# Kernel optimization log

Hardware: AMD Instinct MI355X
Metric: run time of the kernel (lower is better)

The kernel has to match this reference:

```python
import jax, jax.numpy as jnp
import numpy as np

NUM_HEADS = 16
EPS = 1e-6

def _ln(x):
    # LayerNorm32: no affine, eps=1e-6, computed in fp32
    x32 = x.astype(jnp.float32)
    mu = x32.mean(-1, keepdims=True)
    var = x32.var(-1, keepdims=True)
    return ((x32 - mu) * jax.lax.rsqrt(var + EPS)).astype(x.dtype)

def setup_inputs() -> dict:
    key = jax.random.key(0)
    ks = jax.random.split(key, 20)
    B, N, T, C = 2, 2048, 256, 1024
    H = 4 * C
    s = 0.02
    inp = {
        "x": jax.random.normal(ks[0], (B, N, C), jnp.float32),
        "mod": jax.random.normal(ks[1], (B, C), jnp.float32),
        "cond": jax.random.normal(ks[2], (B, T, C), jnp.float32),
        # adaLN: SiLU -> Linear(C, 6C)
        "w_adaln": jax.random.normal(ks[3], (C, 6 * C), jnp.float32) * s,
        "b_adaln": jnp.zeros((6 * C,), jnp.float32),
        # attention qkv + out proj
        "w_qkv": jax.random.normal(ks[4], (C, 3 * C), jnp.float32) * s,
        "b_qkv": jnp.zeros((3 * C,), jnp.float32),
        "w_proj": jax.random.normal(ks[5], (C, C), jnp.float32) * s,
        "b_proj": jnp.zeros((C,), jnp.float32),
        # sparse-branch MLP (GELU tanh)
        "w_s1": jax.random.normal(ks[6], (C, H), jnp.float32) * s,
        "b_s1": jnp.zeros((H,), jnp.float32),
        "w_s2": jax.random.normal(ks[7], (H, C), jnp.float32) * s,
        "b_s2": jnp.zeros((C,), jnp.float32),
        # dense cond MLP (SiLU)
        "w_d1": jax.random.normal(ks[8], (C, H), jnp.float32) * s,
        "b_d1": jnp.zeros((H,), jnp.float32),
        "w_d2": jax.random.normal(ks[9], (H, C), jnp.float32) * s,
        "b_d2": jnp.zeros((C,), jnp.float32),
    }
    return inp

def reference(x, mod, cond, w_adaln, b_adaln, w_qkv, b_qkv, w_proj, b_proj,
              w_s1, b_s1, w_s2, b_s2, w_d1, b_d1, w_d2, b_d2):
    B, N, C = x.shape
    T = cond.shape[1]
    D = C // NUM_HEADS

    # adaLN-zero modulation: [B, 6C] -> six [B, C]
    m = jax.nn.silu(mod) @ w_adaln + b_adaln
    sh_msa, sc_msa, g_msa, sh_mlp, sc_mlp, g_mlp = jnp.split(m, 6, axis=-1)

    # LN + (1+scale)*x + shift on both branches
    x_adaln = _ln(x) * (1.0 + sc_msa[:, None]) + sh_msa[:, None]
    c_adaln = _ln(cond) * (1.0 + sc_msa[:, None]) + sh_msa[:, None]

    # joint tokens per batch: [B, S, C], S = N + T (x tokens first, then cond)
    joint = jnp.concatenate([x_adaln, c_adaln], axis=1)
    S = N + T

    # full multi-head self-attention over the joint sequence
    qkv = joint @ w_qkv + b_qkv                       # [B, S, 3C]
    qkv = qkv.reshape(B, S, 3, NUM_HEADS, D)
    q, k, v = qkv[:, :, 0], qkv[:, :, 1], qkv[:, :, 2]  # [B, S, H, D]
    scores = jnp.einsum('bshd,bthd->bhst', q, k) / jnp.sqrt(jnp.asarray(D, q.dtype))
    attn = jax.nn.softmax(scores, axis=-1)
    out = jnp.einsum('bhst,bthd->bshd', attn, v).reshape(B, S, C)
    out = out @ w_proj + b_proj

    x_attn, c_attn = out[:, :N], out[:, N:]
    x = x + x_attn * g_msa[:, None]
    cond = cond + c_attn * g_msa[:, None]

    # sparse-branch MLP with adaLN (GELU tanh)
    x2 = _ln(x) * (1.0 + sc_mlp[:, None]) + sh_mlp[:, None]
    x2 = jax.nn.gelu(x2 @ w_s1 + b_s1, approximate=True) @ w_s2 + b_s2
    x = x + x2 * g_mlp[:, None]

    # dense cond MLP with adaLN (SiLU)
    c2 = _ln(cond) * (1.0 + sc_mlp[:, None]) + sh_mlp[:, None]
    c2 = jax.nn.silu(c2 @ w_d1 + b_d1) @ w_d2 + b_d2
    cond = cond + c2 * g_mlp[:, None]

    return (x, cond)
```

## Files before the change

kernel.cpp:

```cpp
#include <hip/hip_runtime.h>

typedef unsigned short u16;
typedef __attribute__((ext_vector_type(8))) short short8;
typedef __attribute__((ext_vector_type(4))) short s4b;
typedef __attribute__((ext_vector_type(4))) float floatx4;

#define S_TOT 2304
#define N_SEQ 2048
#define T_SEQ 256
#define C_DIM 1024
#define NH 16
#define DH 64
#define SIX_C 6144

__device__ __forceinline__ u16 f2bf(float f) {
  union { float f; unsigned u; } v; v.f = f;
  unsigned r = (v.u + 0x7FFFu + ((v.u >> 16) & 1u)) >> 16;
  return (u16)r;
}
__device__ __forceinline__ float bf2f(u16 u) {
  union { unsigned u; float f; } v; v.u = ((unsigned)u) << 16; return v.f;
}
__device__ __forceinline__ unsigned fbits(float f) {
  union { float f; unsigned u; } v; v.f = f; return v.u;
}

__device__ __forceinline__ void async16(const void* g, void* l) {
  __builtin_amdgcn_global_load_lds((const __attribute__((address_space(1))) void*)g,
                                   (__attribute__((address_space(3))) void*)l, 16, 0, 0);
}

__device__ __forceinline__ floatx4 zero4() {
  floatx4 z; z[0] = 0.f; z[1] = 0.f; z[2] = 0.f; z[3] = 0.f; return z;
}

__global__ __launch_bounds__(256)
void adaln_mod(const float* __restrict__ mod, const float* __restrict__ w,
               float* __restrict__ m) {
  __shared__ float sm[128];
  int b = blockIdx.y, kz = blockIdx.z;
  int tid = threadIdx.x;
  if (tid < 128) {
    float v = mod[b * C_DIM + kz * 128 + tid];
    sm[tid] = v / (1.f + __expf(-v));
  }
  __syncthreads();
  int j = blockIdx.x * 256 + tid;
  const float* wp = w + (size_t)(kz * 128) * SIX_C + j;
  float acc = 0.f;
  #pragma unroll 8
  for (int k = 0; k < 128; k++) acc += sm[k] * wp[(size_t)k * SIX_C];
  atomicAdd(&m[b * SIX_C + j], acc);
}

__global__ __launch_bounds__(256)
void wtrans_all(const float* __restrict__ w0, const float* __restrict__ w1,
                const float* __restrict__ w2, const float* __restrict__ w3,
                const float* __restrict__ w4, const float* __restrict__ w5,
                u16* __restrict__ o0, u16* __restrict__ o1, u16* __restrict__ o2,
                u16* __restrict__ o3, u16* __restrict__ o4, u16* __restrict__ o5) {
  int bid = blockIdx.x;
  const float* W; u16* Wt; int K, N, bx, local;
  if (bid < 3072)       { W = w0; Wt = o0; K = 1024; N = 3072; bx = 96;  local = bid; }
  else if (bid < 4096)  { W = w1; Wt = o1; K = 1024; N = 1024; bx = 32;  local = bid - 3072; }
  else if (bid < 8192)  { W = w2; Wt = o2; K = 1024; N = 4096; bx = 128; local = bid - 4096; }
  else if (bid < 12288) { W = w3; Wt = o3; K = 4096; N = 1024; bx = 32;  local = bid - 8192; }
  else if (bid < 16384) { W = w4; Wt = o4; K = 1024; N = 4096; bx = 128; local = bid - 12288; }
  else                  { W = w5; Wt = o5; K = 4096; N = 1024; bx = 32;  local = bid - 16384; }
  int n0 = (local % bx) << 5, k0 = (local / bx) << 5;
  __shared__ float t[32][33];
  int tx = threadIdx.x & 31, ty = threadIdx.x >> 5;
  #pragma unroll
  for (int i = 0; i < 32; i += 8)
    t[ty + i][tx] = W[(size_t)(k0 + ty + i) * N + n0 + tx];
  __syncthreads();
  #pragma unroll
  for (int i = 0; i < 32; i += 8)
    Wt[(size_t)(n0 + ty + i) * K + k0 + tx] = f2bf(t[tx][ty + i]);
}

__global__ __launch_bounds__(256)
void vtrans(const u16* __restrict__ V, u16* __restrict__ Vt) {
  __shared__ u16 t[64][65];
  int s0 = blockIdx.x << 6;
  int bh = blockIdx.y;
  const u16* src = V + (size_t)bh * S_TOT * DH;
  u16* dst = Vt + (size_t)bh * DH * S_TOT;
  int tid = threadIdx.x;
  #pragma unroll
  for (int i = 0; i < 16; i++) {
    int idx = tid + i * 256; int r = idx >> 6, c = idx & 63;
    t[r][c] = src[(size_t)(s0 + r) * DH + c];
  }
  __syncthreads();
  #pragma unroll
  for (int i = 0; i < 16; i++) {
    int idx = tid + i * 256; int r = idx >> 6, c = idx & 63;
    dst[(size_t)r * S_TOT + s0 + c] = t[c][r];
  }
}

template<int SHIFT_OFS>
__global__ __launch_bounds__(256)
void ln_mod(const float* __restrict__ xin, const float* __restrict__ cin,
            const float* __restrict__ m, const float* __restrict__ ba,
            u16* __restrict__ xo, u16* __restrict__ co, u16* __restrict__ joint) {
  int row = blockIdx.x;
  int b = row / S_TOT, s = row - b * S_TOT;
  bool isx = (s < N_SEQ);
  size_t roff = isx ? (((size_t)(b * N_SEQ + s)) << 10)
                    : (((size_t)(b * T_SEQ + (s - N_SEQ))) << 10);
  const float* src = isx ? (xin + roff) : (cin + roff);
  int tid = threadIdx.x;
  float4 v = ((const float4*)src)[tid];
  float s1 = v.x + v.y + v.z + v.w;
  float s2 = v.x * v.x + v.y * v.y + v.z * v.z + v.w * v.w;
  #pragma unroll
  for (int o = 32; o; o >>= 1) { s1 += __shfl_xor(s1, o); s2 += __shfl_xor(s2, o); }
  __shared__ float red[8];
  int wv = tid >> 6, ln = tid & 63;
  if (ln == 0) { red[wv] = s1; red[4 + wv] = s2; }
  __syncthreads();
  s1 = red[0] + red[1] + red[2] + red[3];
  s2 = red[4] + red[5] + red[6] + red[7];
  float mu = s1 * (1.f / 1024.f);
  float var = s2 * (1.f / 1024.f) - mu * mu;
  float rstd = rsqrtf(var + 1e-6f);
  int c = tid << 2;
  const float* mb = m + b * SIX_C;
  float4 sc = *(const float4*)(mb + SHIFT_OFS + 1024 + c);
  float4 sb = *(const float4*)(ba + SHIFT_OFS + 1024 + c);
  float4 sh = *(const float4*)(mb + SHIFT_OFS + c);
  float4 hb = *(const float4*)(ba + SHIFT_OFS + c);
  float y0 = (v.x - mu) * rstd * (1.f + sc.x + sb.x) + sh.x + hb.x;
  float y1 = (v.y - mu) * rstd * (1.f + sc.y + sb.y) + sh.y + hb.y;
  float y2 = (v.z - mu) * rstd * (1.f + sc.z + sb.z) + sh.z + hb.z;
  float y3 = (v.w - mu) * rstd * (1.f + sc.w + sb.w) + sh.w + hb.w;
  unsigned long long o = (unsigned long long)f2bf(y0)
      | ((unsigned long long)f2bf(y1) << 16)
      | ((unsigned long long)f2bf(y2) << 32)
      | ((unsigned long long)f2bf(y3) << 48);
  u16* dst;
  if (SHIFT_OFS == 0) dst = joint + (((size_t)row) << 10);
  else dst = (isx ? xo : co) + roff;
  *(unsigned long long*)(dst + c) = o;
}

template<int MODE, int MT>
__global__ __launch_bounds__(256)
void gemm_k(const u16* __restrict__ A, const u16* __restrict__ Bt,
            const float* __restrict__ bias, int K,
            const float* __restrict__ mvec, const float* __restrict__ ba,
            const float* __restrict__ rx, const float* __restrict__ rc,
            float* __restrict__ ox, float* __restrict__ oc,
            u16* __restrict__ oq, u16* __restrict__ okd, u16* __restrict__ ov)
{
  __shared__ alignas(16) u16 lA[MT * 32];
  __shared__ alignas(16) u16 lB[128 * 32];
  int tid = threadIdx.x;
  int wave = tid >> 6, lane = tid & 63, quad = lane >> 4, l15 = lane & 15;
  int bx = blockIdx.x, by = blockIdx.y;
  const int MF = MT / 32;
  int wm = (wave >> 1) * (MT / 2), wn = (wave & 1) << 6;
  const u16* Ag = A + (size_t)(by * MT) * K;
  const u16* Bg = Bt + (size_t)(bx << 7) * K;
  floatx4 acc[MF][4];
  #pragma unroll
  for (int i = 0; i < MF; i++)
    #pragma unroll
    for (int j = 0; j < 4; j++) acc[i][j] = zero4();

  for (int k0 = 0; k0 < K; k0 += 32) {
    #pragma unroll
    for (int i = 0; i < MT / 64; i++) {
      int c = tid + (i << 8);
      async16(&Ag[(size_t)(c >> 2) * K + k0 + ((c & 3) << 3)], &lA[(size_t)c << 3]);
    }
    #pragma unroll
    for (int i = 0; i < 2; i++) {
      int c = tid + (i << 8);
      async16(&Bg[(size_t)(c >> 2) * K + k0 + ((c & 3) << 3)], &lB[(size_t)c << 3]);
    }
    __syncthreads();
    short8 af[MF], bfr[4];
    #pragma unroll
    for (int i = 0; i < MF; i++)
      af[i] = *(const short8*)&lA[(wm + (i << 4) + l15) * 32 + (quad << 3)];
    #pragma unroll
    for (int i = 0; i < 4; i++)
      bfr[i] = *(const short8*)&lB[(wn + (i << 4) + l15) * 32 + (quad << 3)];
    #pragma unroll
    for (int mi = 0; mi < MF; mi++)
      #pragma unroll
      for (int ni = 0; ni < 4; ni++)
        acc[mi][ni] = __builtin_amdgcn_mfma_f32_16x16x32_bf16(af[mi], bfr[ni], acc[mi][ni], 0, 0, 0);
    __syncthreads();
  }

  #pragma unroll
  for (int mi = 0; mi < MF; mi++) {
    #pragma unroll
    for (int r = 0; r < 4; r++) {
      int rg = by * MT + wm + (mi << 4) + (quad << 2) + r;
      int b = rg / S_TOT; int s = rg - b * S_TOT;
      if (MODE == 0) {
        #pragma unroll
        for (int ni = 0; ni < 4; ni++) {
          int col = (bx << 7) + wn + (ni << 4) + l15;
          float val = acc[mi][ni][r] + bias[col];
          int part = col >> 10, h = (col >> 6) & 15, d = col & 63;
          u16* dst = (part == 0) ? oq : (part == 1 ? okd : ov);
          dst[(((size_t)(b * NH + h)) * S_TOT + s) * DH + d] = f2bf(val);
        }
      } else {
        #pragma unroll
        for (int ni = 0; ni < 4; ni++) {
          int col = (bx << 7) + wn + (ni << 4) + l15;
          float val = acc[mi][ni][r] + bias[col];
          float g = mvec[b * SIX_C + 2048 + col] + ba[2048 + col];
          if (s < N_SEQ) {
            size_t idx = (((size_t)(b * N_SEQ + s)) << 10) + col;
            ox[idx] = rx[idx] + val * g;
          } else {
            size_t idx = (((size_t)(b * T_SEQ + (s - N_SEQ))) << 10) + col;
            oc[idx] = rc[idx] + val * g;
          }
        }
      }
    }
  }
}

__global__ __launch_bounds__(256)
void mlp1(const u16* __restrict__ Ax, const u16* __restrict__ Ac,
          const u16* __restrict__ Bx, const u16* __restrict__ Bc,
          const float* __restrict__ biasx, const float* __restrict__ biasc,
          u16* __restrict__ h1) {
  bool isx = (blockIdx.y < 32);
  const u16* A = isx ? (Ax + (size_t)(blockIdx.y << 7) * 1024)
                     : (Ac + (size_t)((blockIdx.y - 32) << 7) * 1024);
  const u16* Bt = isx ? Bx : Bc;
  const float* bias = isx ? biasx : biasc;
  const int K = 1024;
  __shared__ alignas(16) u16 lA[128 * 32];
  __shared__ alignas(16) u16 lB[128 * 32];
  int tid = threadIdx.x;
  int wave = tid >> 6, lane = tid & 63, quad = lane >> 4, l15 = lane & 15;
  int bx = blockIdx.x;
  int wm = (wave >> 1) << 6, wn = (wave & 1) << 6;
  const u16* Bg = Bt + (size_t)(bx << 7) * K;
  floatx4 acc[4][4];
  #pragma unroll
  for (int i = 0; i < 4; i++)
    #pragma unroll
    for (int j = 0; j < 4; j++) acc[i][j] = zero4();

  for (int k0 = 0; k0 < K; k0 += 32) {
    #pragma unroll
    for (int i = 0; i < 2; i++) {
      int c = tid + (i << 8);
      async16(&A[(size_t)(c >> 2) * K + k0 + ((c & 3) << 3)], &lA[(size_t)c << 3]);
      async16(&Bg[(size_t)(c >> 2) * K + k0 + ((c & 3) << 3)], &lB[(size_t)c << 3]);
    }
    __syncthreads();
    short8 af[4], bfr[4];
    #pragma unroll
    for (int i = 0; i < 4; i++) {
      af[i]  = *(const short8*)&lA[(wm + (i << 4) + l15) * 32 + (quad << 3)];
      bfr[i] = *(const short8*)&lB[(wn + (i << 4) + l15) * 32 + (quad << 3)];
    }
    #pragma unroll
    for (int mi = 0; mi < 4; mi++)
      #pragma unroll
      for (int ni = 0; ni < 4; ni++)
        acc[mi][ni] = __builtin_amdgcn_mfma_f32_16x16x32_bf16(af[mi], bfr[ni], acc[mi][ni], 0, 0, 0);
    __syncthreads();
  }

  #pragma unroll
  for (int mi = 0; mi < 4; mi++) {
    #pragma unroll
    for (int r = 0; r < 4; r++) {
      int rg = (blockIdx.y << 7) + wm + (mi << 4) + (quad << 2) + r;
      #pragma unroll
      for (int ni = 0; ni < 4; ni++) {
        int col = (bx << 7) + wn + (ni << 4) + l15;
        float t = acc[mi][ni][r] + bias[col];
        float act;
        if (isx) {
          float u = 0.7978845608028654f * (t + 0.044715f * t * t * t);
          float e = __expf(2.f * u);
          act = 0.5f * t * (1.f + (1.f - 2.f / (e + 1.f)));
        } else {
          act = t / (1.f + __expf(-t));
        }
        h1[(size_t)rg * 4096 + col] = f2bf(act);
      }
    }
  }
}

__global__ __launch_bounds__(256)
void mlp2(const u16* __restrict__ h1,
          const u16* __restrict__ Bx, const u16* __restrict__ Bc,
          const float* __restrict__ biasx, const float* __restrict__ biasc,
          const float* __restrict__ mvec, const float* __restrict__ ba,
          float* __restrict__ outx, float* __restrict__ outc) {
  bool isx = (blockIdx.y < 32);
  const u16* A = h1 + (size_t)(blockIdx.y << 7) * 4096;
  const u16* Bt = isx ? Bx : Bc;
  const float* bias = isx ? biasx : biasc;
  const int K = 4096;
  __shared__ alignas(16) u16 lA[128 * 32];
  __shared__ alignas(16) u16 lB[128 * 32];
  int tid = threadIdx.x;
  int wave = tid >> 6, lane = tid & 63, quad = lane >> 4, l15 = lane & 15;
  int bx = blockIdx.x;
  int wm = (wave >> 1) << 6, wn = (wave & 1) << 6;
  const u16* Bg = Bt + (size_t)(bx << 7) * K;
  floatx4 acc[4][4];
  #pragma unroll
  for (int i = 0; i < 4; i++)
    #pragma unroll
    for (int j = 0; j < 4; j++) acc[i][j] = zero4();

  int kn = K >> 1;
  int kbeg = blockIdx.z * kn, kend = kbeg + kn;
  for (int k0 = kbeg; k0 < kend; k0 += 32) {
    #pragma unroll
    for (int i = 0; i < 2; i++) {
      int c = tid + (i << 8);
      async16(&A[(size_t)(c >> 2) * K + k0 + ((c & 3) << 3)], &lA[(size_t)c << 3]);
      async16(&Bg[(size_t)(c >> 2) * K + k0 + ((c & 3) << 3)], &lB[(size_t)c << 3]);
    }
    __syncthreads();
    short8 af[4], bfr[4];
    #pragma unroll
    for (int i = 0; i < 4; i++) {
      af[i]  = *(const short8*)&lA[(wm + (i << 4) + l15) * 32 + (quad << 3)];
      bfr[i] = *(const short8*)&lB[(wn + (i << 4) + l15) * 32 + (quad << 3)];
    }
    #pragma unroll
    for (int mi = 0; mi < 4; mi++)
      #pragma unroll
      for (int ni = 0; ni < 4; ni++)
        acc[mi][ni] = __builtin_amdgcn_mfma_f32_16x16x32_bf16(af[mi], bfr[ni], acc[mi][ni], 0, 0, 0);
    __syncthreads();
  }

  #pragma unroll
  for (int mi = 0; mi < 4; mi++) {
    #pragma unroll
    for (int r = 0; r < 4; r++) {
      int rg = (blockIdx.y << 7) + wm + (mi << 4) + (quad << 2) + r;
      int rl = isx ? rg : (rg - 4096);
      int b = isx ? (rg >> 11) : (rl >> 8);
      float* dst = isx ? outx : outc;
      #pragma unroll
      for (int ni = 0; ni < 4; ni++) {
        int col = (bx << 7) + wn + (ni << 4) + l15;
        float val = acc[mi][ni][r] + (blockIdx.z == 0 ? bias[col] : 0.f);
        float g = mvec[b * SIX_C + 5120 + col] + ba[5120 + col];
        atomicAdd(&dst[(((size_t)rl) << 10) + col], val * g);
      }
    }
  }
}

__global__ __launch_bounds__(256)
void flash_attn(const u16* __restrict__ Q, const u16* __restrict__ K,
                const u16* __restrict__ V, u16* __restrict__ Op,
                float2* __restrict__ ml) {
  __shared__ alignas(16) u16 lK[128 * 64];
  __shared__ alignas(16) u16 lV[64 * 128];
  int tid = threadIdx.x;
  int wave = tid >> 6, lane = tid & 63, quad = lane >> 4, l15 = lane & 15;
  int q0 = blockIdx.x << 7;
  int bh = blockIdx.y;
  int z = blockIdx.z;
  const u16* Qb = Q + (size_t)bh * S_TOT * DH;
  const u16* Kb = K + (size_t)bh * S_TOT * DH;
  const u16* Vb = V + (size_t)bh * DH * S_TOT;

  short8 qf[2][2];
  #pragma unroll
  for (int mi = 0; mi < 2; mi++) {
    const u16* qrow = Qb + (size_t)(q0 + wave * 32 + mi * 16 + l15) * DH;
    #pragma unroll
    for (int kd = 0; kd < 2; kd++) {
      short8 raw = *(const short8*)&qrow[kd * 32 + quad * 8];
      short8 sc;
      #pragma unroll
      for (int j = 0; j < 8; j++) sc[j] = (short)f2bf(bf2f((u16)raw[j]) * 0.125f);
      qf[mi][kd] = sc;
    }
  }

  floatx4 oacc[2][4];
  #pragma unroll
  for (int mi = 0; mi < 2; mi++)
    #pragma unroll
    for (int dt = 0; dt < 4; dt++) oacc[mi][dt] = zero4();
  float mst[2] = {-1e30f, -1e30f}, lst[2] = {0.f, 0.f};

  int kvbeg = z * 768, kvend = kvbeg + 768;
  for (int kv0 = kvbeg; kv0 < kvend; kv0 += 128) {
    #pragma unroll
    for (int i = 0; i < 4; i++) {
      int ci = tid + (i << 8);
      int rK = ci >> 3, clK = ci & 7;
      int cgK = clK ^ (rK & 7);
      async16(&Kb[(size_t)(kv0 + rK) * DH + (cgK << 3)], &lK[(size_t)ci << 3]);
      int rV = ci >> 4, clV = ci & 15;
      int cgV = (clV & 8) | ((clV ^ (rV & 7)) & 7);
      async16(&Vb[(size_t)rV * S_TOT + kv0 + (cgV << 3)], &lV[(size_t)ci << 3]);
    }
    __syncthreads();

    floatx4 sacc[2][8];
    #pragma unroll
    for (int mi = 0; mi < 2; mi++)
      #pragma unroll
      for (int si = 0; si < 8; si++) sacc[mi][si] = zero4();
    #pragma unroll
    for (int si = 0; si < 8; si++) {
      int r = si * 16 + l15;
      #pragma unroll
      for (int kd = 0; kd < 2; kd++) {
        int c = (kd << 2) + quad;
        int cl = c ^ (r & 7);
        short8 kf = *(const short8*)&lK[r * 64 + (cl << 3)];
        sacc[0][si] = __builtin_amdgcn_mfma_f32_16x16x32_bf16(kf, qf[0][kd], sacc[0][si], 0, 0, 0);
        sacc[1][si] = __builtin_amdgcn_mfma_f32_16x16x32_bf16(kf, qf[1][kd], sacc[1][si], 0, 0, 0);
      }
    }

    #pragma unroll
    for (int mi = 0; mi < 2; mi++) {
      float rm = -1e30f;
      #pragma unroll
      for (int si = 0; si < 8; si++)
        #pragma unroll
        for (int r = 0; r < 4; r++) rm = fmaxf(rm, sacc[mi][si][r]);
      rm = fmaxf(rm, __shfl_xor(rm, 16));
      rm = fmaxf(rm, __shfl_xor(rm, 32));
      float mnew = fmaxf(mst[mi], rm);
      float al = __expf(mst[mi] - mnew);
      mst[mi] = mnew;
      float rs = 0.f;
      #pragma unroll
      for (int si = 0; si < 8; si++)
        #pragma unroll
        for (int r = 0; r < 4; r++) {
          float p = __expf(sacc[mi][si][r] - mnew);
          sacc[mi][si][r] = p;
          rs += p;
        }
      rs += __shfl_xor(rs, 16);
      rs += __shfl_xor(rs, 32);
      lst[mi] = lst[mi] * al + rs;
      #pragma unroll
      for (int dt = 0; dt < 4; dt++)
        #pragma unroll
        for (int r = 0; r < 4; r++) oacc[mi][dt][r] *= al;
    }

    #pragma unroll
    for (int si = 0; si < 8; si++) {
      s4b pb[2];
      #pragma unroll
      for (int mi = 0; mi < 2; mi++) {
        union { s4b v; unsigned u[2]; } p;
        p.u[0] = __builtin_amdgcn_perm(fbits(sacc[mi][si][1]), fbits(sacc[mi][si][0]), 0x07060302u);
        p.u[1] = __builtin_amdgcn_perm(fbits(sacc[mi][si][3]), fbits(sacc[mi][si][2]), 0x07060302u);
        pb[mi] = p.v;
      }
      #pragma unroll
      for (int dt = 0; dt < 4; dt++) {
        int r = dt * 16 + l15;
        int c = (si << 1) + (quad >> 1);
        int cl = (c & 8) | ((c ^ (r & 7)) & 7);
        s4b vf = *(const s4b*)&lV[r * 128 + (cl << 3) + ((quad & 1) << 2)];
        oacc[0][dt] = __builtin_amdgcn_mfma_f32_16x16x16bf16_1k(vf, pb[0], oacc[0][dt], 0, 0, 0);
        oacc[1][dt] = __builtin_amdgcn_mfma_f32_16x16x16bf16_1k(vf, pb[1], oacc[1][dt], 0, 0, 0);
      }
    }
    __syncthreads();
  }

  u16* Ob = Op + (size_t)(z * 32 + bh) * S_TOT * DH;
  float2* mlb = ml + (size_t)(z * 32 + bh) * S_TOT;
  #pragma unroll
  for (int mi = 0; mi < 2; mi++) {
    int qg = q0 + wave * 32 + mi * 16 + l15;
    size_t base = (size_t)qg * DH;
    #pragma unroll
    for (int dt = 0; dt < 4; dt++) {
      s4b o;
      #pragma unroll
      for (int r = 0; r < 4; r++) o[r] = (short)f2bf(oacc[mi][dt][r]);
      *(s4b*)&Ob[base + dt * 16 + quad * 4] = o;
    }
    if (quad == 0) mlb[qg] = make_float2(mst[mi], lst[mi]);
  }
}

__global__ __launch_bounds__(256)
void attn_combine(const u16* __restrict__ Op, const float2* __restrict__ ml,
                  u16* __restrict__ O) {
  int tid = threadIdx.x;
  int row = blockIdx.x * 4 + (tid >> 6);
  int d = tid & 63;
  const size_t ZS = (size_t)32 * S_TOT;
  float2 a0 = ml[row], a1 = ml[ZS + row], a2 = ml[2 * ZS + row];
  float M = fmaxf(a0.x, fmaxf(a1.x, a2.x));
  float w0 = __expf(a0.x - M), w1 = __expf(a1.x - M), w2 = __expf(a2.x - M);
  float L = w0 * a0.y + w1 * a1.y + w2 * a2.y;
  size_t stride = ZS * DH;
  size_t idx = (size_t)row * DH + d;
  float o = w0 * bf2f(Op[idx]) + w1 * bf2f(Op[stride + idx]) + w2 * bf2f(Op[2 * stride + idx]);
  o /= L;
  int bh = row / S_TOT, q = row - bh * S_TOT;
  int b = bh >> 4, h = bh & 15;
  O[(((size_t)(b * S_TOT + q)) << 10) + h * 64 + d] = f2bf(o);
}

extern "C" void kernel_launch(void* const* d_in, const int* in_sizes, int n_in,
                              void* d_out, int out_size, void* d_ws, size_t ws_size,
                              hipStream_t stream) {
  const float* x       = (const float*)d_in[0];
  const float* mod     = (const float*)d_in[1];
  const float* cond    = (const float*)d_in[2];
  const float* w_adaln = (const float*)d_in[3];
  const float* b_adaln = (const float*)d_in[4];
  const float* w_qkv   = (const float*)d_in[5];
  const float* b_qkv   = (const float*)d_in[6];
  const float* w_proj  = (const float*)d_in[7];
  const float* b_proj  = (const float*)d_in[8];
  const float* w_s1    = (const float*)d_in[9];
  const float* b_s1    = (const float*)d_in[10];
  const float* w_s2    = (const float*)d_in[11];
  const float* b_s2    = (const float*)d_in[12];
  const float* w_d1    = (const float*)d_in[13];
  const float* b_d1    = (const float*)d_in[14];
  const float* w_d2    = (const float*)d_in[15];
  const float* b_d2    = (const float*)d_in[16];

  float* outx = (float*)d_out;
  float* outc = outx + (size_t)2 * N_SEQ * C_DIM;

  char* w = (char*)d_ws;
  auto alloc = [&](size_t bytes) { char* p = w; w += (bytes + 255) & ~(size_t)255; return p; };
  float* m_ws  = (float*)alloc(12288 * 4);
  u16* wqkvT   = (u16*)alloc((size_t)3072 * 1024 * 2);
  u16* wprojT  = (u16*)alloc((size_t)1024 * 1024 * 2);
  u16* ws1T    = (u16*)alloc((size_t)4096 * 1024 * 2);
  u16* ws2T    = (u16*)alloc((size_t)4096 * 1024 * 2);
  u16* wd1T    = (u16*)alloc((size_t)4096 * 1024 * 2);
  u16* wd2T    = (u16*)alloc((size_t)4096 * 1024 * 2);
  u16* joint   = (u16*)alloc((size_t)4608 * 1024 * 2);
  u16* Qb      = (u16*)alloc((size_t)4718592 * 2);
  u16* Kb      = (u16*)alloc((size_t)4718592 * 2);
  u16* Vb      = (u16*)alloc((size_t)4718592 * 2);
  u16* Vtb     = (u16*)alloc((size_t)4718592 * 2);
  u16* h1      = (u16*)alloc((size_t)4608 * 4096 * 2);
  u16* xln2 = Qb;
  u16* cln2 = Kb;
  u16* attn_out = joint;
  u16* O_part = h1;
  float2* ml = (float2*)(h1 + (size_t)3 * 32 * S_TOT * DH);

  size_t needed = (size_t)(w - (char*)d_ws);
  if (needed > ws_size) {
    hipMemsetAsync(d_out, 0, (size_t)out_size * 4, stream);
    return;
  }

  hipMemsetAsync(m_ws, 0, 12288 * 4, stream);
  adaln_mod<<<dim3(24, 2, 8), 256, 0, stream>>>(mod, w_adaln, m_ws);

  wtrans_all<<<20480, 256, 0, stream>>>(w_qkv, w_proj, w_s1, w_s2, w_d1, w_d2,
                                        wqkvT, wprojT, ws1T, ws2T, wd1T, wd2T);

  ln_mod<0><<<4608, 256, 0, stream>>>(x, cond, m_ws, b_adaln, nullptr, nullptr, joint);

  gemm_k<0, 128><<<dim3(24, 36), 256, 0, stream>>>(joint, wqkvT, b_qkv, 1024,
      nullptr, nullptr, nullptr, nullptr, nullptr, nullptr, Qb, Kb, Vb);

  vtrans<<<dim3(36, 32), 256, 0, stream>>>(Vb, Vtb);
  flash_attn<<<dim3(18, 32, 3), 256, 0, stream>>>(Qb, Kb, Vtb, O_part, ml);
  attn_combine<<<18432, 256, 0, stream>>>(O_part, ml, attn_out);

  gemm_k<1, 64><<<dim3(8, 72), 256, 0, stream>>>(attn_out, wprojT, b_proj, 1024,
      m_ws, b_adaln, x, cond, outx, outc, nullptr, nullptr, nullptr);

  ln_mod<3072><<<4608, 256, 0, stream>>>(outx, outc, m_ws, b_adaln, xln2, cln2, nullptr);

  mlp1<<<dim3(32, 36), 256, 0, stream>>>(xln2, cln2, ws1T, wd1T, b_s1, b_d1, h1);
  mlp2<<<dim3(8, 36, 2), 256, 0, stream>>>(h1, ws2T, wd2T, b_s2, b_d2,
                                           m_ws, b_adaln, outx, outc);
}
```

Baseline: 532.2 us.

## Use exp2 softmax in attention and drop split-K atomics in MLP down-projection

The flash attention kernel now folds log2(e) into the query scale so it can use a native exp2 instead of exp. It packs P to bf16 right after exponentiation and adds an occupancy hint of 3 blocks per CU. The second MLP GEMM replaces its 2-way split-K with atomic adds by 64-row tiles over the full K, writing results with a plain read-modify-write. This removes atomic traffic and the duplicate epilogue, at the cost of smaller tiles with less reuse per block and a longer K loop. The combine kernel also switches to exp2, which stays consistent because the stored row maxima are now in log2 units.

```diff
diff --git a/kernel.cpp b/kernel.cpp
--- a/kernel.cpp
+++ b/kernel.cpp
@@ -23,6 +23,13 @@
 }
 __device__ __forceinline__ unsigned fbits(float f) {
   union { float f; unsigned u; } v; v.f = f; return v.u;
+}
+__device__ __forceinline__ float fexp2(float x) {
+#if __has_builtin(__builtin_amdgcn_exp2f)
+  return __builtin_amdgcn_exp2f(x);
+#else
+  return __expf(x * 0.6931471805599453f);
+#endif
 }
 
 __device__ __forceinline__ void async16(const void* g, void* l) {
@@ -306,42 +313,44 @@
           const float* __restrict__ biasx, const float* __restrict__ biasc,
           const float* __restrict__ mvec, const float* __restrict__ ba,
           float* __restrict__ outx, float* __restrict__ outc) {
-  bool isx = (blockIdx.y < 32);
-  const u16* A = h1 + (size_t)(blockIdx.y << 7) * 4096;
+  bool isx = (blockIdx.y < 64);
+  const u16* A = h1 + (size_t)(blockIdx.y << 6) * 4096;
   const u16* Bt = isx ? Bx : Bc;
   const float* bias = isx ? biasx : biasc;
   const int K = 4096;
-  __shared__ alignas(16) u16 lA[128 * 32];
+  __shared__ alignas(16) u16 lA[64 * 32];
   __shared__ alignas(16) u16 lB[128 * 32];
   int tid = threadIdx.x;
   int wave = tid >> 6, lane = tid & 63, quad = lane >> 4, l15 = lane & 15;
   int bx = blockIdx.x;
-  int wm = (wave >> 1) << 6, wn = (wave & 1) << 6;
+  int wm = (wave >> 1) << 5, wn = (wave & 1) << 6;
   const u16* Bg = Bt + (size_t)(bx << 7) * K;
-  floatx4 acc[4][4];
-  #pragma unroll
-  for (int i = 0; i < 4; i++)
+  floatx4 acc[2][4];
+  #pragma unroll
+  for (int i = 0; i < 2; i++)
     #pragma unroll
     for (int j = 0; j < 4; j++) acc[i][j] = zero4();
 
-  int kn = K >> 1;
-  int kbeg = blockIdx.z * kn, kend = kbeg + kn;
-  for (int k0 = kbeg; k0 < kend; k0 += 32) {
+  for (int k0 = 0; k0 < K; k0 += 32) {
+    {
+      int c = tid;
+      async16(&A[(size_t)(c >> 2) * K + k0 + ((c & 3) << 3)], &lA[(size_t)c << 3]);
+    }
     #pragma unroll
     for (int i = 0; i < 2; i++) {
       int c = tid + (i << 8);
-      async16(&A[(size_t)(c >> 2) * K + k0 + ((c & 3) << 3)], &lA[(size_t)c << 3]);
       async16(&Bg[(size_t)(c >> 2) * K + k0 + ((c & 3) << 3)], &lB[(size_t)c << 3]);
     }
     __syncthreads();
-    short8 af[4], bfr[4];
-    #pragma unroll
-    for (int i = 0; i < 4; i++) {
-      af[i]  = *(const short8*)&lA[(wm + (i << 4) + l15) * 32 + (quad << 3)];
+    short8 af[2], bfr[4];
+    #pragma unroll
+    for (int i = 0; i < 2; i++)
+      af[i] = *(const short8*)&lA[(wm + (i << 4) + l15) * 32 + (quad << 3)];
+    #pragma unroll
+    for (int i = 0; i < 4; i++)
       bfr[i] = *(const short8*)&lB[(wn + (i << 4) + l15) * 32 + (quad << 3)];
-    }
-    #pragma unroll
-    for (int mi = 0; mi < 4; mi++)
+    #pragma unroll
+    for (int mi = 0; mi < 2; mi++)
       #pragma unroll
       for (int ni = 0; ni < 4; ni++)
         acc[mi][ni] = __builtin_amdgcn_mfma_f32_16x16x32_bf16(af[mi], bfr[ni], acc[mi][ni], 0, 0, 0);
@@ -349,25 +358,26 @@
   }
 
   #pragma unroll
-  for (int mi = 0; mi < 4; mi++) {
+  for (int mi = 0; mi < 2; mi++) {
     #pragma unroll
     for (int r = 0; r < 4; r++) {
-      int rg = (blockIdx.y << 7) + wm + (mi << 4) + (quad << 2) + r;
+      int rg = (blockIdx.y << 6) + wm + (mi << 4) + (quad << 2) + r;
       int rl = isx ? rg : (rg - 4096);
       int b = isx ? (rg >> 11) : (rl >> 8);
       float* dst = isx ? outx : outc;
       #pragma unroll
       for (int ni = 0; ni < 4; ni++) {
         int col = (bx << 7) + wn + (ni << 4) + l15;
-        float val = acc[mi][ni][r] + (blockIdx.z == 0 ? bias[col] : 0.f);
+        float val = acc[mi][ni][r] + bias[col];
         float g = mvec[b * SIX_C + 5120 + col] + ba[5120 + col];
-        atomicAdd(&dst[(((size_t)rl) << 10) + col], val * g);
+        size_t idx = (((size_t)rl) << 10) + col;
+        dst[idx] = dst[idx] + val * g;
       }
     }
   }
 }
 
-__global__ __launch_bounds__(256)
+__global__ __launch_bounds__(256, 3)
 void flash_attn(const u16* __restrict__ Q, const u16* __restrict__ K,
                 const u16* __restrict__ V, u16* __restrict__ Op,
                 float2* __restrict__ ml) {
@@ -391,7 +401,7 @@
       short8 raw = *(const short8*)&qrow[kd * 32 + quad * 8];
       short8 sc;
       #pragma unroll
-      for (int j = 0; j < 8; j++) sc[j] = (short)f2bf(bf2f((u16)raw[j]) * 0.125f);
+      for (int j = 0; j < 8; j++) sc[j] = (short)f2bf(bf2f((u16)raw[j]) * 0.1803368801111244f);
       qf[mi][kd] = sc;
     }
   }
@@ -435,6 +445,7 @@
       }
     }
 
+    unsigned pu[2][8][2];
     #pragma unroll
     for (int mi = 0; mi < 2; mi++) {
       float rm = -1e30f;
@@ -445,17 +456,19 @@
       rm = fmaxf(rm, __shfl_xor(rm, 16));
       rm = fmaxf(rm, __shfl_xor(rm, 32));
       float mnew = fmaxf(mst[mi], rm);
-      float al = __expf(mst[mi] - mnew);
+      float al = fexp2(mst[mi] - mnew);
       mst[mi] = mnew;
       float rs = 0.f;
       #pragma unroll
-      for (int si = 0; si < 8; si++)
-        #pragma unroll
-        for (int r = 0; r < 4; r++) {
-          float p = __expf(sacc[mi][si][r] - mnew);
-          sacc[mi][si][r] = p;
-          rs += p;
-        }
+      for (int si = 0; si < 8; si++) {
+        float p0 = fexp2(sacc[mi][si][0] - mnew);
+        float p1 = fexp2(sacc[mi][si][1] - mnew);
+        float p2 = fexp2(sacc[mi][si][2] - mnew);
+        float p3 = fexp2(sacc[mi][si][3] - mnew);
+        rs += (p0 + p1) + (p2 + p3);
+        pu[mi][si][0] = __builtin_amdgcn_perm(fbits(p1), fbits(p0), 0x07060302u);
+        pu[mi][si][1] = __builtin_amdgcn_perm(fbits(p3), fbits(p2), 0x07060302u);
+      }
       rs += __shfl_xor(rs, 16);
       rs += __shfl_xor(rs, 32);
       lst[mi] = lst[mi] * al + rs;
@@ -467,22 +480,17 @@
 
     #pragma unroll
     for (int si = 0; si < 8; si++) {
-      s4b pb[2];
-      #pragma unroll
-      for (int mi = 0; mi < 2; mi++) {
-        union { s4b v; unsigned u[2]; } p;
-        p.u[0] = __builtin_amdgcn_perm(fbits(sacc[mi][si][1]), fbits(sacc[mi][si][0]), 0x07060302u);
-        p.u[1] = __builtin_amdgcn_perm(fbits(sacc[mi][si][3]), fbits(sacc[mi][si][2]), 0x07060302u);
-        pb[mi] = p.v;
-      }
+      union { s4b v; unsigned u[2]; } pb0, pb1;
+      pb0.u[0] = pu[0][si][0]; pb0.u[1] = pu[0][si][1];
+      pb1.u[0] = pu[1][si][0]; pb1.u[1] = pu[1][si][1];
       #pragma unroll
       for (int dt = 0; dt < 4; dt++) {
         int r = dt * 16 + l15;
         int c = (si << 1) + (quad >> 1);
         int cl = (c & 8) | ((c ^ (r & 7)) & 7);
         s4b vf = *(const s4b*)&lV[r * 128 + (cl << 3) + ((quad & 1) << 2)];
-        oacc[0][dt] = __builtin_amdgcn_mfma_f32_16x16x16bf16_1k(vf, pb[0], oacc[0][dt], 0, 0, 0);
-        oacc[1][dt] = __builtin_amdgcn_mfma_f32_16x16x16bf16_1k(vf, pb[1], oacc[1][dt], 0, 0, 0);
+        oacc[0][dt] = __builtin_amdgcn_mfma_f32_16x16x16bf16_1k(vf, pb0.v, oacc[0][dt], 0, 0, 0);
+        oacc[1][dt] = __builtin_amdgcn_mfma_f32_16x16x16bf16_1k(vf, pb1.v, oacc[1][dt], 0, 0, 0);
       }
     }
     __syncthreads();
@@ -514,7 +522,7 @@
   const size_t ZS = (size_t)32 * S_TOT;
   float2 a0 = ml[row], a1 = ml[ZS + row], a2 = ml[2 * ZS + row];
   float M = fmaxf(a0.x, fmaxf(a1.x, a2.x));
-  float w0 = __expf(a0.x - M), w1 = __expf(a1.x - M), w2 = __expf(a2.x - M);
+  float w0 = fexp2(a0.x - M), w1 = fexp2(a1.x - M), w2 = fexp2(a2.x - M);
   float L = w0 * a0.y + w1 * a1.y + w2 * a2.y;
   size_t stride = ZS * DH;
   size_t idx = (size_t)row * DH + d;
@@ -597,6 +605,6 @@
   ln_mod<3072><<<4608, 256, 0, stream>>>(outx, outc, m_ws, b_adaln, xln2, cln2, nullptr);
 
   mlp1<<<dim3(32, 36), 256, 0, stream>>>(xln2, cln2, ws1T, wd1T, b_s1, b_d1, h1);
-  mlp2<<<dim3(8, 36, 2), 256, 0, stream>>>(h1, ws2T, wd2T, b_s2, b_d2,
-                                           m_ws, b_adaln, outx, outc);
-}
+  mlp2<<<dim3(8, 72), 256, 0, stream>>>(h1, ws2T, wd2T, b_s2, b_d2,
+                                        m_ws, b_adaln, outx, outc);
+}
```

Measured after the change: 607.0 us. 1.14x slower.
